# Optimization experiments

Hardware: AMD Instinct MI355X
Metric: run time of the kernel (lower is better)

## Reference

```python
import jax, jax.numpy as jnp
import numpy as np

C_M, C_Z, C, N_HEAD = 256, 128, 32, 8
N_SEQ, N_RES = 256, 256
LN_EPS = 1e-5


def _layer_norm(x, w, b):
    mu = jnp.mean(x, axis=-1, keepdims=True)
    var = jnp.var(x, axis=-1, keepdims=True)
    return (x - mu) * jax.lax.rsqrt(var + LN_EPS) * w + b


def setup_inputs() -> dict:
    key = jax.random.key(0)
    ks = jax.random.split(key, 12)
    s = 0.02
    return {
        "m": jax.random.normal(ks[0], (N_SEQ, N_RES, C_M), dtype=jnp.float32),
        "z": jax.random.normal(ks[1], (N_RES, N_RES, C_Z), dtype=jnp.float32),
        "ln_m_w": jnp.ones((C_M,), jnp.float32),
        "ln_m_b": jnp.zeros((C_M,), jnp.float32),
        "ln_z_w": jnp.ones((C_Z,), jnp.float32),
        "ln_z_b": jnp.zeros((C_Z,), jnp.float32),
        "Wz": jax.random.normal(ks[2], (C_Z, N_HEAD), dtype=jnp.float32) * s,
        "Wq": jax.random.normal(ks[3], (C_M, N_HEAD * C), dtype=jnp.float32) * s,
        "Wk": jax.random.normal(ks[4], (C_M, N_HEAD * C), dtype=jnp.float32) * s,
        "Wv": jax.random.normal(ks[5], (C_M, N_HEAD * C), dtype=jnp.float32) * s,
        "Wg": jax.random.normal(ks[6], (C_M, N_HEAD * C), dtype=jnp.float32) * s,
        "bg": jnp.zeros((N_HEAD * C,), jnp.float32),
        "Wo": jax.random.normal(ks[7], (N_HEAD * C, C_M), dtype=jnp.float32) * s,
        "bo": jnp.zeros((C_M,), jnp.float32),
    }


def reference(m, z, ln_m_w, ln_m_b, ln_z_w, ln_z_b, Wz, Wq, Wk, Wv, Wg, bg, Wo, bo):
    S, R, cm = m.shape
    mn = _layer_norm(m, ln_m_w, ln_m_b)            # (S, R, c_m)
    zn = _layer_norm(z, ln_z_w, ln_z_b)            # (R, R, c_z)
    bias = jnp.einsum('qkz,zh->hqk', zn, Wz)       # (H, R, R), pair bias per head

    Wqh = Wq.reshape(cm, N_HEAD, C)
    Wkh = Wk.reshape(cm, N_HEAD, C)
    Wvh = Wv.reshape(cm, N_HEAD, C)
    q = jnp.einsum('srm,mhc->shrc', mn, Wqh)       # (S, H, R, c)
    k = jnp.einsum('srm,mhc->shrc', mn, Wkh)
    v = jnp.einsum('srm,mhc->shrc', mn, Wvh)

    scale = 1.0 / jnp.sqrt(jnp.asarray(C, mn.dtype))
    scores = jnp.einsum('shqc,shkc->shqk', q, k) * scale + bias[None]  # (S, H, R, R)
    attn = jax.nn.softmax(scores, axis=-1)
    o = jnp.einsum('shqk,shkc->shqc', attn, v)     # (S, H, R, c)
    o = o.transpose(0, 2, 1, 3).reshape(S, R, N_HEAD * C)

    g = jax.nn.sigmoid(mn @ Wg + bg)               # gating, (S, R, H*c)
    return (g * o) @ Wo + bo                       # (S, R, c_m)
```

## Files before the change

kernel.cpp:

```cpp
#include <hip/hip_runtime.h>
#include <cmath>

#define NSEQ 256
#define NRES 256
#define CM   256
#define CZ   128
#define NHEAD 8
#define CHD  32
#define NROW 65536

typedef __attribute__((ext_vector_type(8))) short short8;
typedef __attribute__((ext_vector_type(4))) short s16x4;
typedef __attribute__((ext_vector_type(4))) float f32x4;

__device__ __forceinline__ unsigned short f2bf(float x) {
    union { float f; unsigned int u; } v; v.f = x;
    unsigned int u = v.u;
    u += 0x7fffu + ((u >> 16) & 1u);
    return (unsigned short)(u >> 16);
}
__device__ __forceinline__ float bf2f(unsigned short b) {
    union { float f; unsigned int u; } v; v.u = ((unsigned int)b) << 16;
    return v.f;
}

__device__ __forceinline__ void async16(const void* g, void* l) {
    __builtin_amdgcn_global_load_lds(
        (const __attribute__((address_space(1))) unsigned int*)g,
        (__attribute__((address_space(3))) unsigned int*)l, 16, 0, 0);
}

__device__ __forceinline__ void xcd_remap(int& x, int& y) {
    const int nx = gridDim.x, ny = gridDim.y;
    const int b = blockIdx.x + blockIdx.y * nx;
    if ((ny & 7) == 0) {
        const int c = b & 7;
        const int t = b >> 3;
        x = t % nx;
        y = c + 8 * (t / nx);
    } else {
        x = blockIdx.x; y = blockIdx.y;
    }
}

__global__ void __launch_bounds__(64)
ln_m_kernel(const float* __restrict__ m, const float* __restrict__ w,
            const float* __restrict__ b, unsigned short* __restrict__ mbf) {
    const int row = blockIdx.x;
    const int t = threadIdx.x;
    const float* x = m + (size_t)row * CM;
    float4 xv = *(const float4*)(x + t * 4);
    float s  = xv.x + xv.y + xv.z + xv.w;
    float s2 = xv.x * xv.x + xv.y * xv.y + xv.z * xv.z + xv.w * xv.w;
#pragma unroll
    for (int off = 32; off > 0; off >>= 1) {
        s  += __shfl_xor(s, off);
        s2 += __shfl_xor(s2, off);
    }
    const float mu  = s * (1.0f / CM);
    const float var = s2 * (1.0f / CM) - mu * mu;
    const float inv = rsqrtf(var + 1e-5f);
    float4 wv = *(const float4*)(w + t * 4);
    float4 bv = *(const float4*)(b + t * 4);
    ushort4 o4;
    o4.x = f2bf((xv.x - mu) * inv * wv.x + bv.x);
    o4.y = f2bf((xv.y - mu) * inv * wv.y + bv.y);
    o4.z = f2bf((xv.z - mu) * inv * wv.z + bv.z);
    o4.w = f2bf((xv.w - mu) * inv * wv.w + bv.w);
    *(ushort4*)(mbf + (size_t)row * CM + t * 4) = o4;
}

__global__ void __launch_bounds__(64)
ln_z_bias_kernel(const float* __restrict__ z, const float* __restrict__ w,
                 const float* __restrict__ b, const float* __restrict__ Wz,
                 float* __restrict__ bias) {
    const int pair = blockIdx.x;
    const int t = threadIdx.x;
    const float* x = z + (size_t)pair * CZ;
    float2 xv = *(const float2*)(x + t * 2);
    float s  = xv.x + xv.y;
    float s2 = xv.x * xv.x + xv.y * xv.y;
#pragma unroll
    for (int off = 32; off > 0; off >>= 1) {
        s  += __shfl_xor(s, off);
        s2 += __shfl_xor(s2, off);
    }
    const float mu  = s * (1.0f / CZ);
    const float var = s2 * (1.0f / CZ) - mu * mu;
    const float inv = rsqrtf(var + 1e-5f);
    float2 wv = *(const float2*)(w + t * 2);
    float2 bv = *(const float2*)(b + t * 2);
    const float zn0 = (xv.x - mu) * inv * wv.x + bv.x;
    const float zn1 = (xv.y - mu) * inv * wv.y + bv.y;
    float ph[NHEAD];
#pragma unroll
    for (int h = 0; h < NHEAD; h++)
        ph[h] = zn0 * Wz[(2 * t) * NHEAD + h] + zn1 * Wz[(2 * t + 1) * NHEAD + h];
#pragma unroll
    for (int h = 0; h < NHEAD; h++) {
#pragma unroll
        for (int off = 32; off > 0; off >>= 1) ph[h] += __shfl_xor(ph[h], off);
    }
    if (t == 0) {
#pragma unroll
        for (int h = 0; h < NHEAD; h++)
            bias[(size_t)h * NROW + pair] = ph[h] * 1.4426950408889634f;
    }
}

__global__ void __launch_bounds__(256)
wsplit_kernel(const float* __restrict__ Wq, const float* __restrict__ Wk,
              const float* __restrict__ Wv, const float* __restrict__ Wg,
              const float* __restrict__ Wo, unsigned short* __restrict__ wbf) {
    const int n = blockIdx.x;
    const int mat = blockIdx.y;
    const int k = threadIdx.x;
    const float* W = (mat == 0) ? Wq : (mat == 1) ? Wk : (mat == 2) ? Wv
                   : (mat == 3) ? Wg : Wo;
    const float v = W[(size_t)k * 256 + n];
    unsigned short h = f2bf(v);
    unsigned short* hi = wbf + (size_t)mat * 65536;
    hi[(size_t)n * 256 + k] = h;
    if (mat == 4) {
        unsigned short* lo = wbf + (size_t)5 * 65536;
        lo[(size_t)n * 256 + k] = f2bf(v - bf2f(h));
    }
}

__global__ void __launch_bounds__(256)
gemm_qkvg_kernel(const unsigned short* __restrict__ A,
                 const unsigned short* __restrict__ wbf,
                 unsigned short* __restrict__ qb, unsigned short* __restrict__ kb,
                 unsigned short* __restrict__ vb, unsigned short* __restrict__ gb,
                 const float* __restrict__ bg, float scale, int rowsTot) {
    __shared__ short LDS[128 * 128];
    short* A_s = LDS;
    short* B_s = LDS + 128 * 64;
    int bx, by;
    xcd_remap(bx, by);
    const int which = bx >> 1;
    const int n0 = (bx & 1) * 128;
    const int m0 = by * 128;
    const unsigned short* Bt_g = wbf + (size_t)which * 65536;
    unsigned short* C = (which == 0) ? qb : (which == 1) ? kb : (which == 2) ? vb : gb;
    const float alpha = (which == 0) ? scale : 1.0f;
    const float* bias = (which == 3) ? bg : nullptr;
    const int act = (which == 3) ? 1 : 0;

    const int tid  = threadIdx.x;
    const int wid  = tid >> 6;
    const int lane = tid & 63;
    const int wm = (wid >> 1) * 64;
    const int wn = (wid & 1) * 64;

    f32x4 acc[4][4];
#pragma unroll
    for (int i = 0; i < 4; i++)
#pragma unroll
        for (int j = 0; j < 4; j++) acc[i][j] = (f32x4){0.f, 0.f, 0.f, 0.f};

    const unsigned short* gmat = (wid < 2) ? A : Bt_g;
    short* lmat = (wid < 2) ? A_s : B_s;
    const int brow = (wid < 2) ? m0 : n0;
    const int half = (wid & 1) * 64;
    const int srow  = lane >> 3;
    const int sslot = (lane & 7) ^ srow;

    const int lrow = lane & 15;
    const int lg   = lane >> 4;
    const int x0 = ((0 + lg) ^ (lane & 7)) * 8;
    const int x1 = ((4 + lg) ^ (lane & 7)) * 8;

    for (int k0 = 0; k0 < 256; k0 += 64) {
#pragma unroll
        for (int r = 0; r < 8; r++) {
            const unsigned short* g = gmat
                + (size_t)(brow + half + r * 8 + srow) * 256 + k0 + sslot * 8;
            short* l = lmat + (half + r * 8) * 64;
            async16(g, l);
        }
        __syncthreads();

#pragma unroll
        for (int kk = 0; kk < 2; kk++) {
            const int x = kk ? x1 : x0;
            short8 af[4], bf[4];
#pragma unroll
            for (int f = 0; f < 4; f++) {
                af[f] = *(const short8*)&A_s[(wm + f * 16 + lrow) * 64 + x];
                bf[f] = *(const short8*)&B_s[(wn + f * 16 + lrow) * 64 + x];
            }
#pragma unroll
            for (int i = 0; i < 4; i++)
#pragma unroll
                for (int j = 0; j < 4; j++)
                    acc[i][j] = __builtin_amdgcn_mfma_f32_16x16x32_bf16(af[i], bf[j], acc[i][j], 0, 0, 0);
        }
        __syncthreads();
    }

    {
        const int ccol0 = lane & 15;
        const int crow0 = lg * 4;
        float bvv[4];
#pragma unroll
        for (int j = 0; j < 4; j++)
            bvv[j] = bias ? bias[n0 + wn + j * 16 + ccol0] : 0.0f;
#pragma unroll
        for (int i = 0; i < 4; i++)
#pragma unroll
            for (int r = 0; r < 4; r++) {
                const int row = wm + i * 16 + crow0 + r;
#pragma unroll
                for (int j = 0; j < 4; j++) {
                    float vv = acc[i][j][r] * alpha + bvv[j];
                    if (act == 1) vv = 1.0f / (1.0f + __expf(-vv));
                    LDS[row * 128 + wn + j * 16 + ccol0] = (short)f2bf(vv);
                }
            }
        __syncthreads();
        const int rr = tid >> 4;
        const int cb = (tid & 15) * 8;
        const int pl = n0 / 32 + (cb >> 5);
        const int cw = cb & 31;
#pragma unroll
        for (int t = 0; t < 8; t++) {
            const int row = t * 16 + rr;
            short8 vv = *(const short8*)&LDS[row * 128 + cb];
            *(short8*)&C[((size_t)pl * rowsTot + m0 + row) * 32 + cw] = vv;
        }
    }
}

__global__ void __launch_bounds__(256)
gemm_out_kernel(const unsigned int* __restrict__ Ap_g,
                const unsigned short* __restrict__ wbf, float* __restrict__ C,
                const float* __restrict__ bo, int rowsTot) {
    __shared__ unsigned int Ap_s[128 * 32];
    __shared__ short Bhi_s[128 * 32];
    __shared__ short Blo_s[128 * 32];
    int bx, by;
    xcd_remap(bx, by);
    const int m0 = by * 128, n0 = bx * 128;
    const unsigned short* Bthi_g = wbf + (size_t)4 * 65536;
    const unsigned short* Btlo_g = wbf + (size_t)5 * 65536;

    const int tid  = threadIdx.x;
    const int wid  = tid >> 6;
    const int lane = tid & 63;
    const int wm = (wid >> 1) * 64;
    const int wn = (wid & 1) * 64;

    f32x4 acc[4][4];
#pragma unroll
    for (int i = 0; i < 4; i++)
#pragma unroll
        for (int j = 0; j < 4; j++) acc[i][j] = (f32x4){0.f, 0.f, 0.f, 0.f};

    const int lrow = lane & 15;
    const int lk   = (lane >> 4) * 8;

    for (int k0 = 0; k0 < 256; k0 += 32) {
        if (wid < 2) {
            const int half = wid * 64;
            const int srow = lane >> 3;
            const int scol = (lane & 7) * 4;
#pragma unroll
            for (int r = 0; r < 8; r++) {
                const unsigned int* g = Ap_g
                    + ((size_t)(k0 >> 5) * rowsTot + m0 + half + r * 8 + srow) * 32 + scol;
                unsigned int* l = Ap_s + (half + r * 8) * 32;
                async16(g, l);
            }
        } else {
            const unsigned short* gmat = (wid == 2) ? Bthi_g : Btlo_g;
            short* lmat = (wid == 2) ? Bhi_s : Blo_s;
            const int srow = lane >> 2;
            const int skq  = (lane & 3) * 8;
#pragma unroll
            for (int r = 0; r < 8; r++) {
                const unsigned short* g = gmat + (size_t)(n0 + r * 16 + srow) * 256 + k0 + skq;
                short* l = lmat + (r * 16) * 32;
                async16(g, l);
            }
        }
        __syncthreads();

        short8 ah[4], al[4], bh[4], bl[4];
#pragma unroll
        for (int f = 0; f < 4; f++) {
            const uint4* ap = (const uint4*)&Ap_s[(wm + f * 16 + lrow) * 32 + lk];
            uint4 a0 = ap[0], a1 = ap[1];
            union { unsigned int u[4]; short8 s; } uh, ul;
            uh.u[0] = __builtin_amdgcn_perm(a0.y, a0.x, 0x07060302u);
            uh.u[1] = __builtin_amdgcn_perm(a0.w, a0.z, 0x07060302u);
            uh.u[2] = __builtin_amdgcn_perm(a1.y, a1.x, 0x07060302u);
            uh.u[3] = __builtin_amdgcn_perm(a1.w, a1.z, 0x07060302u);
            ul.u[0] = __builtin_amdgcn_perm(a0.y, a0.x, 0x05040100u);
            ul.u[1] = __builtin_amdgcn_perm(a0.w, a0.z, 0x05040100u);
            ul.u[2] = __builtin_amdgcn_perm(a1.y, a1.x, 0x05040100u);
            ul.u[3] = __builtin_amdgcn_perm(a1.w, a1.z, 0x05040100u);
            ah[f] = uh.s; al[f] = ul.s;
            bh[f] = *(const short8*)&Bhi_s[(wn + f * 16 + lrow) * 32 + lk];
            bl[f] = *(const short8*)&Blo_s[(wn + f * 16 + lrow) * 32 + lk];
        }
#pragma unroll
        for (int i = 0; i < 4; i++)
#pragma unroll
            for (int j = 0; j < 4; j++) {
                acc[i][j] = __builtin_amdgcn_mfma_f32_16x16x32_bf16(ah[i], bh[j], acc[i][j], 0, 0, 0);
                acc[i][j] = __builtin_amdgcn_mfma_f32_16x16x32_bf16(ah[i], bl[j], acc[i][j], 0, 0, 0);
                acc[i][j] = __builtin_amdgcn_mfma_f32_16x16x32_bf16(al[i], bh[j], acc[i][j], 0, 0, 0);
            }
        __syncthreads();
    }

    const int ccol0 = lane & 15;
    const int crow0 = (lane >> 4) * 4;
    float bvv[4];
#pragma unroll
    for (int j = 0; j < 4; j++)
        bvv[j] = bo[n0 + wn + j * 16 + ccol0];
#pragma unroll
    for (int i = 0; i < 4; i++) {
#pragma unroll
        for (int r = 0; r < 4; r++) {
            const int row = m0 + wm + i * 16 + crow0 + r;
#pragma unroll
            for (int j = 0; j < 4; j++) {
                const int col = n0 + wn + j * 16 + ccol0;
                C[(size_t)row * 256 + col] = acc[i][j][r] + bvv[j];
            }
        }
    }
}

__global__ void __launch_bounds__(256, 4)
attn_mfma_kernel(const unsigned short* __restrict__ q, const unsigned short* __restrict__ k,
                 const unsigned short* __restrict__ v, const float* __restrict__ bias_qk,
                 const unsigned short* __restrict__ g,
                 unsigned int* __restrict__ opack, int rows) {
    const int s = blockIdx.x, h = blockIdx.y;
    __shared__ short Ks[256][40];
    __shared__ short Vs[32][268];
    __shared__ float li_s[4][64];
    const int tid = threadIdx.x;
    const int w = tid >> 6, l = tid & 63;
    const int lg = l >> 4, l15 = l & 15;
    const size_t hb = ((size_t)h * rows + (size_t)s * NRES) * 32;

    {
        const int kk0 = tid >> 2;
        const int c8 = (tid & 3) * 8;
#pragma unroll
        for (int r4 = 0; r4 < 4; r4++) {
            const int kk = r4 * 64 + kk0;
            const size_t gi = hb + (size_t)kk * 32 + c8;
            short8 k8 = *(const short8*)(k + gi);
            short8 v8 = *(const short8*)(v + gi);
            *(short8*)&Ks[kk][c8] = k8;
#pragma unroll
            for (int jj = 0; jj < 8; jj++) Vs[c8 + jj][kk] = v8[jj];
        }
    }
    const int wq0 = w * 64;
    short8 qf[4];
#pragma unroll
    for (int mq = 0; mq < 4; mq++)
        qf[mq] = *(const short8*)(q + hb + (size_t)(wq0 + mq * 16 + l15) * 32 + lg * 8);
    __syncthreads();

    f32x4 acco[4][2];
#pragma unroll
    for (int mq = 0; mq < 4; mq++)
#pragma unroll
        for (int nc = 0; nc < 2; nc++) acco[mq][nc] = (f32x4){0.f, 0.f, 0.f, 0.f};
    float lip[4] = {0.f, 0.f, 0.f, 0.f};
    const float* bh = bias_qk + (size_t)h * NROW;

    for (int ch = 0; ch < 8; ch++) {
        const int kb = ch * 32;
        short8 kf[2];
#pragma unroll
        for (int ik = 0; ik < 2; ik++)
            kf[ik] = *(const short8*)&Ks[kb + ik * 16 + l15][lg * 8];
#pragma unroll
        for (int ik = 0; ik < 2; ik++) {
            s16x4 vf[2];
#pragma unroll
            for (int nc = 0; nc < 2; nc++)
                vf[nc] = *(const s16x4*)&Vs[nc * 16 + l15][kb + ik * 16 + lg * 4];
            const int kkr = ik * 16 + lg * 4;
#pragma unroll
            for (int jq = 0; jq < 4; jq++) {
                const int qrow = wq0 + jq * 16 + l15;
                f32x4 sa = (f32x4){0.f, 0.f, 0.f, 0.f};
                sa = __builtin_amdgcn_mfma_f32_16x16x32_bf16(kf[ik], qf[jq], sa, 0, 0, 0);
                float4 bv = *(const float4*)(bh + (size_t)qrow * NRES + kb + kkr);
                const float p0 = __builtin_amdgcn_exp2f(sa[0] + bv.x);
                const float p1 = __builtin_amdgcn_exp2f(sa[1] + bv.y);
                const float p2 = __builtin_amdgcn_exp2f(sa[2] + bv.z);
                const float p3 = __builtin_amdgcn_exp2f(sa[3] + bv.w);
                lip[jq] += (p0 + p1) + (p2 + p3);
                s16x4 pa;
                pa[0] = (short)f2bf(p0); pa[1] = (short)f2bf(p1);
                pa[2] = (short)f2bf(p2); pa[3] = (short)f2bf(p3);
#pragma unroll
                for (int nc = 0; nc < 2; nc++)
                    acco[jq][nc] = __builtin_amdgcn_mfma_f32_16x16x16bf16_1k(
                        pa, vf[nc], acco[jq][nc], 0, 0, 0);
            }
        }
    }

#pragma unroll
    for (int jq = 0; jq < 4; jq++) {
        lip[jq] += __shfl_xor(lip[jq], 16);
        lip[jq] += __shfl_xor(lip[jq], 32);
        li_s[w][jq * 16 + l15] = lip[jq];
    }

#pragma unroll
    for (int mq = 0; mq < 4; mq++) {
#pragma unroll
        for (int r = 0; r < 4; r++) {
            const int qrow = wq0 + mq * 16 + lg * 4 + r;
            const float inv = 1.0f / li_s[w][mq * 16 + lg * 4 + r];
            const size_t rb = hb + (size_t)qrow * 32;
#pragma unroll
            for (int nc = 0; nc < 2; nc++) {
                const int c = nc * 16 + l15;
                const float val = acco[mq][nc][r] * inv * bf2f(g[rb + c]);
                const unsigned short hi = f2bf(val);
                const unsigned short lo = f2bf(val - bf2f(hi));
                opack[rb + c] = ((unsigned int)hi << 16) | lo;
            }
        }
    }
}

extern "C" void kernel_launch(void* const* d_in, const int* in_sizes, int n_in,
                              void* d_out, int out_size, void* d_ws, size_t ws_size,
                              hipStream_t stream) {
    const float* m    = (const float*)d_in[0];
    const float* z    = (const float*)d_in[1];
    const float* lnmw = (const float*)d_in[2];
    const float* lnmb = (const float*)d_in[3];
    const float* lnzw = (const float*)d_in[4];
    const float* lnzb = (const float*)d_in[5];
    const float* Wz   = (const float*)d_in[6];
    const float* Wq   = (const float*)d_in[7];
    const float* Wk   = (const float*)d_in[8];
    const float* Wv   = (const float*)d_in[9];
    const float* Wg   = (const float*)d_in[10];
    const float* bg   = (const float*)d_in[11];
    const float* Wo   = (const float*)d_in[12];
    const float* bo   = (const float*)d_in[13];
    float* out = (float*)d_out;

    char* wsb = (char*)d_ws;
    const size_t BIASB = (size_t)NHEAD * NROW * 4;
    const size_t WBFB  = (size_t)6 * 65536 * 2;
    float* bias_qk = (float*)wsb;
    unsigned short* wbf = (unsigned short*)(wsb + BIASB);
    char* chunk0 = wsb + BIASB + ((WBFB + 255) & ~(size_t)255);

    const size_t avail = ws_size - (size_t)(chunk0 - wsb);
    int SC = NSEQ;
    while (SC > 1 && (size_t)SC * NRES * CM * 14 > avail) SC >>= 1;
    const size_t CHE = (size_t)SC * NRES * CM;

    unsigned short* qb  = (unsigned short*)chunk0;
    unsigned short* kb  = qb + CHE;
    unsigned short* vb  = kb + CHE;
    unsigned short* gb  = vb + CHE;
    unsigned short* mbf = gb + CHE;
    unsigned int* opk   = (unsigned int*)(mbf + CHE);

    ln_z_bias_kernel<<<NROW, 64, 0, stream>>>(z, lnzw, lnzb, Wz, bias_qk);
    wsplit_kernel<<<dim3(256, 5), 256, 0, stream>>>(Wq, Wk, Wv, Wg, Wo, wbf);

    const int rows = SC * NRES;
    const int mtiles = rows / 128;
    const float scale = 0.17677669529663687f * 1.4426950408889634f;

    for (int s0 = 0; s0 < NSEQ; s0 += SC) {
        const float* m_c   = m   + (size_t)s0 * NRES * CM;
        float*       out_c = out + (size_t)s0 * NRES * CM;

        ln_m_kernel<<<rows, 64, 0, stream>>>(m_c, lnmw, lnmb, mbf);

        gemm_qkvg_kernel<<<dim3(8, mtiles), 256, 0, stream>>>(
            mbf, wbf, qb, kb, vb, gb, bg, scale, rows);

        attn_mfma_kernel<<<dim3(SC, NHEAD), 256, 0, stream>>>(
            qb, kb, vb, bias_qk, gb, opk, rows);

        gemm_out_kernel<<<dim3(2, mtiles), 256, 0, stream>>>(
            opk, wbf, out_c, bo, rows);
    }
}
```

Measured before the change: 370.0 us.

## Use plain bf16 for output projection and prefetch pair bias in attention

Result: faster. 347.6 us (-6.1%).

```diff
diff --git a/kernel.cpp b/kernel.cpp
--- a/kernel.cpp
+++ b/kernel.cpp
@@ -118,13 +118,8 @@
     const float* W = (mat == 0) ? Wq : (mat == 1) ? Wk : (mat == 2) ? Wv
                    : (mat == 3) ? Wg : Wo;
     const float v = W[(size_t)k * 256 + n];
-    unsigned short h = f2bf(v);
     unsigned short* hi = wbf + (size_t)mat * 65536;
-    hi[(size_t)n * 256 + k] = h;
-    if (mat == 4) {
-        unsigned short* lo = wbf + (size_t)5 * 65536;
-        lo[(size_t)n * 256 + k] = f2bf(v - bf2f(h));
-    }
+    hi[(size_t)n * 256 + k] = f2bf(v);
 }
 
 __global__ void __launch_bounds__(256)
@@ -233,17 +228,16 @@
 }
 
 __global__ void __launch_bounds__(256)
-gemm_out_kernel(const unsigned int* __restrict__ Ap_g,
+gemm_out_kernel(const unsigned short* __restrict__ A,
                 const unsigned short* __restrict__ wbf, float* __restrict__ C,
                 const float* __restrict__ bo, int rowsTot) {
-    __shared__ unsigned int Ap_s[128 * 32];
-    __shared__ short Bhi_s[128 * 32];
-    __shared__ short Blo_s[128 * 32];
+    __shared__ short LDS[128 * 128];
+    short* A_s = LDS;
+    short* B_s = LDS + 128 * 64;
     int bx, by;
     xcd_remap(bx, by);
     const int m0 = by * 128, n0 = bx * 128;
-    const unsigned short* Bthi_g = wbf + (size_t)4 * 65536;
-    const unsigned short* Btlo_g = wbf + (size_t)5 * 65536;
+    const unsigned short* Bt_g = wbf + (size_t)4 * 65536;
 
     const int tid  = threadIdx.x;
     const int wid  = tid >> 6;
@@ -257,66 +251,54 @@
 #pragma unroll
         for (int j = 0; j < 4; j++) acc[i][j] = (f32x4){0.f, 0.f, 0.f, 0.f};
 
+    const int half = (wid & 1) * 64;
+    const int srow  = lane >> 3;
+    const int sslot = (lane & 7) ^ srow;
+
     const int lrow = lane & 15;
-    const int lk   = (lane >> 4) * 8;
-
-    for (int k0 = 0; k0 < 256; k0 += 32) {
-        if (wid < 2) {
-            const int half = wid * 64;
-            const int srow = lane >> 3;
-            const int scol = (lane & 7) * 4;
-#pragma unroll
-            for (int r = 0; r < 8; r++) {
-                const unsigned int* g = Ap_g
-                    + ((size_t)(k0 >> 5) * rowsTot + m0 + half + r * 8 + srow) * 32 + scol;
-                unsigned int* l = Ap_s + (half + r * 8) * 32;
+    const int lg   = lane >> 4;
+    const int x0 = ((0 + lg) ^ (lane & 7)) * 8;
+    const int x1 = ((4 + lg) ^ (lane & 7)) * 8;
+
+    for (int k0 = 0; k0 < 256; k0 += 64) {
+#pragma unroll
+        for (int r = 0; r < 8; r++) {
+            if (wid < 2) {
+                const int row = m0 + half + r * 8 + srow;
+                const unsigned short* g = A
+                    + ((size_t)((k0 >> 5) + (sslot >> 2)) * rowsTot + row) * 32
+                    + (sslot & 3) * 8;
+                short* l = A_s + (half + r * 8) * 64;
                 async16(g, l);
-            }
-        } else {
-            const unsigned short* gmat = (wid == 2) ? Bthi_g : Btlo_g;
-            short* lmat = (wid == 2) ? Bhi_s : Blo_s;
-            const int srow = lane >> 2;
-            const int skq  = (lane & 3) * 8;
-#pragma unroll
-            for (int r = 0; r < 8; r++) {
-                const unsigned short* g = gmat + (size_t)(n0 + r * 16 + srow) * 256 + k0 + skq;
-                short* l = lmat + (r * 16) * 32;
+            } else {
+                const unsigned short* g = Bt_g
+                    + (size_t)(n0 + half + r * 8 + srow) * 256 + k0 + sslot * 8;
+                short* l = B_s + (half + r * 8) * 64;
                 async16(g, l);
             }
         }
         __syncthreads();
 
-        short8 ah[4], al[4], bh[4], bl[4];
-#pragma unroll
-        for (int f = 0; f < 4; f++) {
-            const uint4* ap = (const uint4*)&Ap_s[(wm + f * 16 + lrow) * 32 + lk];
-            uint4 a0 = ap[0], a1 = ap[1];
-            union { unsigned int u[4]; short8 s; } uh, ul;
-            uh.u[0] = __builtin_amdgcn_perm(a0.y, a0.x, 0x07060302u);
-            uh.u[1] = __builtin_amdgcn_perm(a0.w, a0.z, 0x07060302u);
-            uh.u[2] = __builtin_amdgcn_perm(a1.y, a1.x, 0x07060302u);
-            uh.u[3] = __builtin_amdgcn_perm(a1.w, a1.z, 0x07060302u);
-            ul.u[0] = __builtin_amdgcn_perm(a0.y, a0.x, 0x05040100u);
-            ul.u[1] = __builtin_amdgcn_perm(a0.w, a0.z, 0x05040100u);
-            ul.u[2] = __builtin_amdgcn_perm(a1.y, a1.x, 0x05040100u);
-            ul.u[3] = __builtin_amdgcn_perm(a1.w, a1.z, 0x05040100u);
-            ah[f] = uh.s; al[f] = ul.s;
-            bh[f] = *(const short8*)&Bhi_s[(wn + f * 16 + lrow) * 32 + lk];
-            bl[f] = *(const short8*)&Blo_s[(wn + f * 16 + lrow) * 32 + lk];
-        }
-#pragma unroll
-        for (int i = 0; i < 4; i++)
-#pragma unroll
-            for (int j = 0; j < 4; j++) {
-                acc[i][j] = __builtin_amdgcn_mfma_f32_16x16x32_bf16(ah[i], bh[j], acc[i][j], 0, 0, 0);
-                acc[i][j] = __builtin_amdgcn_mfma_f32_16x16x32_bf16(ah[i], bl[j], acc[i][j], 0, 0, 0);
-                acc[i][j] = __builtin_amdgcn_mfma_f32_16x16x32_bf16(al[i], bh[j], acc[i][j], 0, 0, 0);
-            }
+#pragma unroll
+        for (int kk = 0; kk < 2; kk++) {
+            const int x = kk ? x1 : x0;
+            short8 af[4], bf[4];
+#pragma unroll
+            for (int f = 0; f < 4; f++) {
+                af[f] = *(const short8*)&A_s[(wm + f * 16 + lrow) * 64 + x];
+                bf[f] = *(const short8*)&B_s[(wn + f * 16 + lrow) * 64 + x];
+            }
+#pragma unroll
+            for (int i = 0; i < 4; i++)
+#pragma unroll
+                for (int j = 0; j < 4; j++)
+                    acc[i][j] = __builtin_amdgcn_mfma_f32_16x16x32_bf16(af[i], bf[j], acc[i][j], 0, 0, 0);
+        }
         __syncthreads();
     }
 
     const int ccol0 = lane & 15;
-    const int crow0 = (lane >> 4) * 4;
+    const int crow0 = lg * 4;
     float bvv[4];
 #pragma unroll
     for (int j = 0; j < 4; j++)
@@ -334,12 +316,41 @@
         }
     }
 }
+
+#define ISSUE_B(DST, KABS) do {                                              \
+    const int ka_ = (KABS);                                                  \
+    _Pragma("unroll")                                                        \
+    for (int jq_ = 0; jq_ < 4; jq_++)                                        \
+        DST[jq_] = *(const float4*)(bh + (size_t)(wq0 + jq_ * 16 + l15) * NRES + ka_); \
+} while (0)
+
+#define PROCESS_IK(KB, IK, BB) do {                                          \
+    const int kb_ = (KB), ik_ = (IK);                                        \
+    short8 kf_ = *(const short8*)&Ks[kb_ + ik_ * 16 + l15][lg * 8];          \
+    s16x4 vf0_ = *(const s16x4*)&Vs[l15][kb_ + ik_ * 16 + lg * 4];           \
+    s16x4 vf1_ = *(const s16x4*)&Vs[16 + l15][kb_ + ik_ * 16 + lg * 4];      \
+    _Pragma("unroll")                                                        \
+    for (int jq_ = 0; jq_ < 4; jq_++) {                                      \
+        f32x4 sa_ = (f32x4){0.f, 0.f, 0.f, 0.f};                             \
+        sa_ = __builtin_amdgcn_mfma_f32_16x16x32_bf16(kf_, qf[jq_], sa_, 0, 0, 0); \
+        const float p0_ = __builtin_amdgcn_exp2f(sa_[0] + BB[jq_].x);        \
+        const float p1_ = __builtin_amdgcn_exp2f(sa_[1] + BB[jq_].y);        \
+        const float p2_ = __builtin_amdgcn_exp2f(sa_[2] + BB[jq_].z);        \
+        const float p3_ = __builtin_amdgcn_exp2f(sa_[3] + BB[jq_].w);        \
+        lip[jq_] += (p0_ + p1_) + (p2_ + p3_);                               \
+        s16x4 pa_;                                                           \
+        pa_[0] = (short)f2bf(p0_); pa_[1] = (short)f2bf(p1_);                \
+        pa_[2] = (short)f2bf(p2_); pa_[3] = (short)f2bf(p3_);                \
+        acco[jq_][0] = __builtin_amdgcn_mfma_f32_16x16x16bf16_1k(pa_, vf0_, acco[jq_][0], 0, 0, 0); \
+        acco[jq_][1] = __builtin_amdgcn_mfma_f32_16x16x16bf16_1k(pa_, vf1_, acco[jq_][1], 0, 0, 0); \
+    }                                                                        \
+} while (0)
 
 __global__ void __launch_bounds__(256, 4)
 attn_mfma_kernel(const unsigned short* __restrict__ q, const unsigned short* __restrict__ k,
                  const unsigned short* __restrict__ v, const float* __restrict__ bias_qk,
                  const unsigned short* __restrict__ g,
-                 unsigned int* __restrict__ opack, int rows) {
+                 unsigned short* __restrict__ obf, int rows) {
     const int s = blockIdx.x, h = blockIdx.y;
     __shared__ short Ks[256][40];
     __shared__ short Vs[32][268];
@@ -378,39 +389,14 @@
     float lip[4] = {0.f, 0.f, 0.f, 0.f};
     const float* bh = bias_qk + (size_t)h * NROW;
 
+    float4 bb0[4], bb1[4];
+    ISSUE_B(bb0, lg * 4);
     for (int ch = 0; ch < 8; ch++) {
         const int kb = ch * 32;
-        short8 kf[2];
-#pragma unroll
-        for (int ik = 0; ik < 2; ik++)
-            kf[ik] = *(const short8*)&Ks[kb + ik * 16 + l15][lg * 8];
-#pragma unroll
-        for (int ik = 0; ik < 2; ik++) {
-            s16x4 vf[2];
-#pragma unroll
-            for (int nc = 0; nc < 2; nc++)
-                vf[nc] = *(const s16x4*)&Vs[nc * 16 + l15][kb + ik * 16 + lg * 4];
-            const int kkr = ik * 16 + lg * 4;
-#pragma unroll
-            for (int jq = 0; jq < 4; jq++) {
-                const int qrow = wq0 + jq * 16 + l15;
-                f32x4 sa = (f32x4){0.f, 0.f, 0.f, 0.f};
-                sa = __builtin_amdgcn_mfma_f32_16x16x32_bf16(kf[ik], qf[jq], sa, 0, 0, 0);
-                float4 bv = *(const float4*)(bh + (size_t)qrow * NRES + kb + kkr);
-                const float p0 = __builtin_amdgcn_exp2f(sa[0] + bv.x);
-                const float p1 = __builtin_amdgcn_exp2f(sa[1] + bv.y);
-                const float p2 = __builtin_amdgcn_exp2f(sa[2] + bv.z);
-                const float p3 = __builtin_amdgcn_exp2f(sa[3] + bv.w);
-                lip[jq] += (p0 + p1) + (p2 + p3);
-                s16x4 pa;
-                pa[0] = (short)f2bf(p0); pa[1] = (short)f2bf(p1);
-                pa[2] = (short)f2bf(p2); pa[3] = (short)f2bf(p3);
-#pragma unroll
-                for (int nc = 0; nc < 2; nc++)
-                    acco[jq][nc] = __builtin_amdgcn_mfma_f32_16x16x16bf16_1k(
-                        pa, vf[nc], acco[jq][nc], 0, 0, 0);
-            }
-        }
+        ISSUE_B(bb1, kb + 16 + lg * 4);
+        PROCESS_IK(kb, 0, bb0);
+        if (ch < 7) ISSUE_B(bb0, kb + 32 + lg * 4);
+        PROCESS_IK(kb, 1, bb1);
     }
 
 #pragma unroll
@@ -431,9 +417,7 @@
             for (int nc = 0; nc < 2; nc++) {
                 const int c = nc * 16 + l15;
                 const float val = acco[mq][nc][r] * inv * bf2f(g[rb + c]);
-                const unsigned short hi = f2bf(val);
-                const unsigned short lo = f2bf(val - bf2f(hi));
-                opack[rb + c] = ((unsigned int)hi << 16) | lo;
+                obf[rb + c] = f2bf(val);
             }
         }
     }
@@ -460,14 +444,14 @@
 
     char* wsb = (char*)d_ws;
     const size_t BIASB = (size_t)NHEAD * NROW * 4;
-    const size_t WBFB  = (size_t)6 * 65536 * 2;
+    const size_t WBFB  = (size_t)5 * 65536 * 2;
     float* bias_qk = (float*)wsb;
     unsigned short* wbf = (unsigned short*)(wsb + BIASB);
     char* chunk0 = wsb + BIASB + ((WBFB + 255) & ~(size_t)255);
 
     const size_t avail = ws_size - (size_t)(chunk0 - wsb);
     int SC = NSEQ;
-    while (SC > 1 && (size_t)SC * NRES * CM * 14 > avail) SC >>= 1;
+    while (SC > 1 && (size_t)SC * NRES * CM * 12 > avail) SC >>= 1;
     const size_t CHE = (size_t)SC * NRES * CM;
 
     unsigned short* qb  = (unsigned short*)chunk0;
@@ -475,7 +459,7 @@
     unsigned short* vb  = kb + CHE;
     unsigned short* gb  = vb + CHE;
     unsigned short* mbf = gb + CHE;
-    unsigned int* opk   = (unsigned int*)(mbf + CHE);
+    unsigned short* obf = mbf + CHE;
 
     ln_z_bias_kernel<<<NROW, 64, 0, stream>>>(z, lnzw, lnzb, Wz, bias_qk);
     wsplit_kernel<<<dim3(256, 5), 256, 0, stream>>>(Wq, Wk, Wv, Wg, Wo, wbf);
@@ -494,9 +478,9 @@
             mbf, wbf, qb, kb, vb, gb, bg, scale, rows);
 
         attn_mfma_kernel<<<dim3(SC, NHEAD), 256, 0, stream>>>(
-            qb, kb, vb, bias_qk, gb, opk, rows);
+            qb, kb, vb, bias_qk, gb, obf, rows);
 
         gemm_out_kernel<<<dim3(2, mtiles), 256, 0, stream>>>(
-            opk, wbf, out_c, bo, rows);
-    }
-}
+            obf, wbf, out_c, bo, rows);
+    }
+}
```
